# Kernel optimization log

Hardware: AMD Instinct MI355X
Metric: run time of the kernel (lower is better)

The kernel has to match this reference:

```python
import jax, jax.numpy as jnp
import numpy as np

HEADS = 8
DHEAD = 64
KSIZE = 7


def setup_inputs() -> dict:
    key = jax.random.key(0)
    k1, k2, k3, k4 = jax.random.split(key, 4)
    b, H, W, C = 16, 56, 56, 256
    inner = HEADS * DHEAD  # 512
    x = jax.random.normal(k1, (b, H, W, C), jnp.float32)
    Wq = jax.random.normal(k2, (1, 1, C, inner), jnp.float32) * 0.02
    Wkv = jax.random.normal(k3, (KSIZE, KSIZE, C, 2 * inner), jnp.float32) * 0.02
    Wo = jax.random.normal(k4, (1, 1, inner, C), jnp.float32) * 0.02
    bo = jnp.zeros((C,), jnp.float32)
    return {"x": x, "Wq": Wq, "Wkv": Wkv, "Wo": Wo, "bo": bo}


def reference(x, Wq, Wkv, Wo, bo):
    heads, dh = HEADS, DHEAD
    scale = dh ** -0.5
    b, H, W, C = x.shape
    # 1x1 conv Q projection == per-pixel matmul
    q = jnp.einsum('bhwc,cf->bhwf', x, Wq[0, 0])  # [b,H,W,inner]
    # k x k strided conv KV downsample (SAME==VALID since H%k==0)
    kv = jax.lax.conv_general_dilated(
        x, Wkv, window_strides=(KSIZE, KSIZE), padding='VALID',
        dimension_numbers=('NHWC', 'HWIO', 'NHWC'))  # [b,H/k,W/k,2*inner]
    k_, v_ = jnp.split(kv, 2, axis=-1)

    def split_heads(t):
        B, hh, ww, _ = t.shape
        return t.reshape(B, hh * ww, heads, dh)  # [b, seq, h, d]

    q = split_heads(q)      # [b, H*W, h, d]
    k_ = split_heads(k_)    # [b, (H/k)*(W/k), h, d]
    v_ = split_heads(v_)
    dots = jnp.einsum('bqhd,bkhd->bhqk', q, k_) * scale
    attn = jax.nn.softmax(dots, axis=-1)
    out = jnp.einsum('bhqk,bkhd->bqhd', attn, v_)
    out = out.reshape(b, H, W, heads * dh)
    # output 1x1 conv with bias (dropout rate 0 -> identity)
    out = jnp.einsum('bhwf,fc->bhwc', out, Wo[0, 0]) + bo
    return out
```

## Files before the change

### kernel.cpp

```cpp
#include <hip/hip_runtime.h>
#include <stdint.h>

typedef unsigned short ushort_t;
typedef __attribute__((ext_vector_type(8))) unsigned short ushort8v;
typedef __attribute__((ext_vector_type(8))) short short8v;
typedef __attribute__((ext_vector_type(4))) float f32x4;

__device__ __forceinline__ float bf2f(ushort_t u) {
  union { unsigned int i; float f; } v;
  v.i = ((unsigned int)u) << 16;
  return v.f;
}
__device__ __forceinline__ ushort_t f2bf(float f) {
  union { float f; unsigned int i; } v;
  v.f = f;
  unsigned int r = v.i + 0x7FFFu + ((v.i >> 16) & 1u);
  return (ushort_t)(r >> 16);
}

__device__ __forceinline__ ushort8v load8bf(const ushort_t* __restrict__ p) {
  return *(const ushort8v*)p;
}
__device__ __forceinline__ ushort8v load8bf(const float* __restrict__ p) {
  const float4 a = *(const float4*)p;
  const float4 b = *(const float4*)(p + 4);
  ushort8v r;
  r[0] = f2bf(a.x); r[1] = f2bf(a.y); r[2] = f2bf(a.z); r[3] = f2bf(a.w);
  r[4] = f2bf(b.x); r[5] = f2bf(b.y); r[6] = f2bf(b.z); r[7] = f2bf(b.w);
  return r;
}
__device__ __forceinline__ void storeC(float* p, float v) { *p = v; }
__device__ __forceinline__ void storeC(ushort_t* p, float v) { *p = f2bf(v); }

__device__ __forceinline__ size_t pp_off(unsigned g) {
  const unsigned b = g / 3136u;
  const unsigned r = g - b * 3136u;
  const unsigned y = r / 56u, xx = r - y * 56u;
  const unsigned ty = y / 7u, dy = y - ty * 7u;
  const unsigned tx = xx / 7u, dx = xx - tx * 7u;
  return ((size_t)((b * 64u + ty * 8u + tx) * 49u + dy * 7u + dx)) << 8;
}

__global__ __launch_bounds__(256) void transpose_cvt(
    const float* __restrict__ W, ushort_t* __restrict__ WT, int K, int N) {
  __shared__ float tile[32][33];
  const int t = threadIdx.x;
  const int k0 = blockIdx.y * 32;
  const int n0 = blockIdx.x * 32;
  {
    const int r = t >> 3, c4 = (t & 7) * 4;
    const float4 v = *(const float4*)(W + (size_t)(k0 + r) * N + n0 + c4);
    tile[r][c4] = v.x; tile[r][c4 + 1] = v.y;
    tile[r][c4 + 2] = v.z; tile[r][c4 + 3] = v.w;
  }
  __syncthreads();
  {
    const int rn = t >> 3, ck = (t & 7) * 4;
    union { ushort_t u[4]; uint2 v; } o;
#pragma unroll
    for (int j = 0; j < 4; ++j) o.u[j] = f2bf(tile[ck + j][rn]);
    *(uint2*)(WT + (size_t)(n0 + rn) * K + k0 + ck) = o.v;
  }
}

__global__ __launch_bounds__(256) void cvt_f32_bf16(
    const float* __restrict__ in, ushort_t* __restrict__ out) {
  const int i = (blockIdx.x * 256 + threadIdx.x) * 4;
  const float4 v = *(const float4*)(in + i);
  union { ushort_t u[4]; uint2 q; } o;
  o.u[0] = f2bf(v.x); o.u[1] = f2bf(v.y);
  o.u[2] = f2bf(v.z); o.u[3] = f2bf(v.w);
  *(uint2*)(out + i) = o.q;
}

__global__ __launch_bounds__(256) void cvt_im2col(
    const float* __restrict__ x, ushort_t* __restrict__ xp) {
  const int e = (blockIdx.x * 256 + threadIdx.x) * 8;
  const unsigned p = ((unsigned)e) >> 8;
  const int c = e & 255;
  const float4 a = *(const float4*)(x + e);
  const float4 b = *(const float4*)(x + e + 4);
  ushort8v o;
  o[0] = f2bf(a.x); o[1] = f2bf(a.y); o[2] = f2bf(a.z); o[3] = f2bf(a.w);
  o[4] = f2bf(b.x); o[5] = f2bf(b.y); o[6] = f2bf(b.z); o[7] = f2bf(b.w);
  *(ushort8v*)(xp + pp_off(p) + c) = o;
}

template <int MODE, bool PERMA>
__device__ __forceinline__ void gemm_body(
    const ushort_t* __restrict__ A, const ushort_t* __restrict__ BT,
    const float* __restrict__ bias, void* __restrict__ Cv,
    int N, int K, int m0, int n0, int kbeg, int kend) {
  __shared__ ushort_t lA[2][4096];
  __shared__ ushort_t lB[2][4096];
  const int t = threadIdx.x;
  const int lane = t & 63;
  const int wv = t >> 6;
  const int wm = wv >> 1, wn = wv & 1;
  const int sm = t >> 2;
  const int kq = t & 3;

  const int row16 = sm & 15;
  const int wslot = kq * 16 + (row16 ^ kq);
  const int rdsw = (lane ^ ((lane >> 4) & 3)) * 8;

  const ushort_t* aR[2];
  const ushort_t* bR[2];
  int off[2];
#pragma unroll
  for (int h = 0; h < 2; ++h) {
    const int m = h * 64 + sm;
    off[h] = (h * 4 + wv) * 512 + wslot * 8;
    size_t aoff;
    if (PERMA)
      aoff = pp_off((unsigned)(m0 + m));
    else
      aoff = (size_t)(m0 + m) * K;
    aR[h] = A + aoff + kq * 8;
    bR[h] = BT + (size_t)(n0 + m) * K + kq * 8;
  }

  f32x4 acc[4][4] = {};
  const int nst = (kend - kbeg) >> 5;

  ushort8v av[2], bv[2];
#pragma unroll
  for (int h = 0; h < 2; ++h) {
    av[h] = *(const ushort8v*)(aR[h] + kbeg);
    bv[h] = *(const ushort8v*)(bR[h] + kbeg);
  }
#pragma unroll
  for (int h = 0; h < 2; ++h) {
    *(ushort8v*)&lA[0][off[h]] = av[h];
    *(ushort8v*)&lB[0][off[h]] = bv[h];
  }
  __syncthreads();

  for (int st = 0; st < nst; ++st) {
    const int cur = st & 1;
    if (st + 1 < nst) {
      const int nk = kbeg + (st + 1) * 32;
#pragma unroll
      for (int h = 0; h < 2; ++h) {
        av[h] = *(const ushort8v*)(aR[h] + nk);
        bv[h] = *(const ushort8v*)(bR[h] + nk);
      }
    }

    short8v af[4], bfr[4];
#pragma unroll
    for (int i = 0; i < 4; ++i) {
      af[i] = *(const short8v*)&lA[cur][(wm * 4 + i) * 512 + rdsw];
      bfr[i] = *(const short8v*)&lB[cur][(wn * 4 + i) * 512 + rdsw];
    }
#pragma unroll
    for (int i = 0; i < 4; ++i)
#pragma unroll
      for (int j = 0; j < 4; ++j)
        acc[i][j] = __builtin_amdgcn_mfma_f32_16x16x32_bf16(
            af[i], bfr[j], acc[i][j], 0, 0, 0);

    if (st + 1 < nst) {
#pragma unroll
      for (int h = 0; h < 2; ++h) {
        *(ushort8v*)&lA[cur ^ 1][off[h]] = av[h];
        *(ushort8v*)&lB[cur ^ 1][off[h]] = bv[h];
      }
    }
    __syncthreads();
  }

  const int col = lane & 15, rq = (lane >> 4) * 4;
#pragma unroll
  for (int i = 0; i < 4; ++i) {
    const int mb = m0 + (wm * 4 + i) * 16 + rq;
#pragma unroll
    for (int j = 0; j < 4; ++j) {
      const int nb = n0 + (wn * 4 + j) * 16 + col;
      if (MODE == 0) {
        ushort_t* C = (ushort_t*)Cv;
#pragma unroll
        for (int r = 0; r < 4; ++r)
          C[(size_t)(mb + r) * N + nb] = f2bf(acc[i][j][r]);
      } else if (MODE == 1) {
        float* C = (float*)Cv;
        const float badd = bias[nb];
#pragma unroll
        for (int r = 0; r < 4; ++r)
          C[(size_t)(mb + r) * N + nb] = acc[i][j][r] + badd;
      } else {
        float* C = (float*)Cv;
#pragma unroll
        for (int r = 0; r < 4; ++r)
          atomicAdd(&C[(size_t)(mb + r) * N + nb], acc[i][j][r]);
      }
    }
  }
}

template <int MODE, bool PERMA>
__global__ __launch_bounds__(256) void gemm_nt_2d(
    const ushort_t* __restrict__ A, const ushort_t* __restrict__ BT,
    const float* __restrict__ bias, void* __restrict__ C, int N, int K) {
  gemm_body<MODE, PERMA>(A, BT, bias, C, N, K, blockIdx.y * 128,
                         blockIdx.x * 128, 0, K);
}

__global__ __launch_bounds__(256) void gemm_kv_gl(
    const ushort_t* __restrict__ xpat, const ushort_t* __restrict__ WkvT,
    float* __restrict__ C) {
  const int bl = blockIdx.x;
  const int kbeg = (bl >> 6) * 896;
  gemm_body<2, false>(xpat, WkvT, (const float*)nullptr, C, 1024, 12544,
                      (bl & 7) * 128, ((bl >> 3) & 7) * 128, kbeg, kbeg + 896);
}

template <typename TA, typename TC>
__global__ __launch_bounds__(256) void gemm_mfma_nt(
    const TA* __restrict__ A, const ushort_t* __restrict__ BT,
    const float* __restrict__ bias, TC* __restrict__ C,
    int M, int N, int K, int has_bias) {
  __shared__ ushort_t lA[8 * 512];
  __shared__ ushort_t lB[8 * 512];
  const int t = threadIdx.x;
  const int m0 = blockIdx.y * 128;
  const int n0 = blockIdx.x * 128;
  const int lane = t & 63;
  const int wm = (t >> 6) >> 1, wn = (t >> 6) & 1;

  f32x4 acc[4][4] = {};

  const int sm = t >> 2;
  const int kq = t & 3;

  for (int k0 = 0; k0 < K; k0 += 32) {
#pragma unroll
    for (int h = 0; h < 2; ++h) {
      const int m = h * 64 + sm;
      const int off = (m >> 4) * 512 + (kq * 16 + (m & 15)) * 8;
      const ushort8v av = load8bf(A + (size_t)(m0 + m) * K + k0 + kq * 8);
      *(ushort8v*)&lA[off] = av;
      const ushort8v bv = load8bf(BT + (size_t)(n0 + m) * K + k0 + kq * 8);
      *(ushort8v*)&lB[off] = bv;
    }
    __syncthreads();
    short8v af[4], bf[4];
#pragma unroll
    for (int i = 0; i < 4; ++i) {
      af[i] = *(const short8v*)&lA[(wm * 4 + i) * 512 + lane * 8];
      bf[i] = *(const short8v*)&lB[(wn * 4 + i) * 512 + lane * 8];
    }
#pragma unroll
    for (int i = 0; i < 4; ++i)
#pragma unroll
      for (int j = 0; j < 4; ++j)
        acc[i][j] = __builtin_amdgcn_mfma_f32_16x16x32_bf16(
            af[i], bf[j], acc[i][j], 0, 0, 0);
    __syncthreads();
  }

  const int col = lane & 15, rq = (lane >> 4) * 4;
#pragma unroll
  for (int i = 0; i < 4; ++i) {
    const int mb = m0 + (wm * 4 + i) * 16 + rq;
#pragma unroll
    for (int j = 0; j < 4; ++j) {
      const int nb = n0 + (wn * 4 + j) * 16 + col;
      const float badd = has_bias ? bias[nb] : 0.f;
#pragma unroll
      for (int r = 0; r < 4; ++r)
        storeC(&C[(size_t)(mb + r) * N + nb], acc[i][j][r] + badd);
    }
  }
}

template <typename TA>
__global__ __launch_bounds__(256) void gemm_kv_mfma(
    const TA* __restrict__ x, const ushort_t* __restrict__ WkvT,
    float* __restrict__ C) {
  __shared__ ushort_t lA[8 * 512];
  __shared__ ushort_t lB[8 * 512];
  const int t = threadIdx.x;
  const int bl = blockIdx.x;
  const int m0 = (bl & 7) * 128;
  const int n0 = ((bl >> 3) & 7) * 128;
  const int kbeg = (bl >> 6) * 896;
  const int lane = t & 63;
  const int wm = (t >> 6) >> 1, wn = (t >> 6) & 1;

  f32x4 acc[4][4] = {};

  const int sm = t >> 2;
  const int kq = t & 3;

  for (int k0 = kbeg; k0 < kbeg + 896; k0 += 32) {
#pragma unroll
    for (int h = 0; h < 2; ++h) {
      const int m = h * 64 + sm;
      const int off = (m >> 4) * 512 + (kq * 16 + (m & 15)) * 8;
      const int gm = m0 + m;
      const int b = gm >> 6, ty = (gm >> 3) & 7, tx = gm & 7;
      const int k = k0 + kq * 8;
      const int patch = k >> 8;
      const int c = k & 255;
      const int dy = (patch * 37) >> 8;
      const int dx = patch - dy * 7;
      const int pix = b * 3136 + (ty * 7 + dy) * 56 + (tx * 7 + dx);
      const ushort8v av = load8bf(x + (size_t)pix * 256 + c);
      *(ushort8v*)&lA[off] = av;
      const ushort8v bv =
          load8bf(WkvT + (size_t)(n0 + m) * 12544 + k0 + kq * 8);
      *(ushort8v*)&lB[off] = bv;
    }
    __syncthreads();
    short8v af[4], bf[4];
#pragma unroll
    for (int i = 0; i < 4; ++i) {
      af[i] = *(const short8v*)&lA[(wm * 4 + i) * 512 + lane * 8];
      bf[i] = *(const short8v*)&lB[(wn * 4 + i) * 512 + lane * 8];
    }
#pragma unroll
    for (int i = 0; i < 4; ++i)
#pragma unroll
      for (int j = 0; j < 4; ++j)
        acc[i][j] = __builtin_amdgcn_mfma_f32_16x16x32_bf16(
            af[i], bf[j], acc[i][j], 0, 0, 0);
    __syncthreads();
  }

  const int col = lane & 15, rq = (lane >> 4) * 4;
#pragma unroll
  for (int i = 0; i < 4; ++i) {
    const int mb = m0 + (wm * 4 + i) * 16 + rq;
#pragma unroll
    for (int j = 0; j < 4; ++j) {
      const int nb = n0 + (wn * 4 + j) * 16 + col;
#pragma unroll
      for (int r = 0; r < 4; ++r)
        atomicAdd(&C[(size_t)(mb + r) * 1024 + nb], acc[i][j][r]);
    }
  }
}

__global__ __launch_bounds__(256) void attn_mfma(
    ushort_t* __restrict__ qo, const ushort_t* __restrict__ kvb) {
  __shared__ ushort_t VT[64][72];
  __shared__ ushort_t P[4][64][72];
  const int t = threadIdx.x;
  const int lane = t & 63;
  const int w = t >> 6;
  const int bh = blockIdx.y;
  const int b = bh >> 3, h = bh & 7;
  const ushort_t* kvp = kvb + (size_t)(b * 64) * 1024 + h * 64;

  for (int i = t; i < 512; i += 256) {
    const int key = i >> 3, d0 = (i & 7) * 8;
    const ushort8v v = *(const ushort8v*)(kvp + (size_t)key * 1024 + 512 + d0);
#pragma unroll
    for (int jj = 0; jj < 8; ++jj) VT[d0 + jj][key] = v[jj];
  }
  __syncthreads();

  const int q0_raw = blockIdx.x * 256 + w * 64;
  const bool valid = q0_raw < 3136;
  const int q0 = valid ? q0_raw : 3072;
  const size_t qbase = ((size_t)b * 3136 + q0) * 512 + h * 64;

  const int lm = lane & 15, quad = lane >> 4;

  short8v qf[4][2], kf[4][2];
#pragma unroll
  for (int i = 0; i < 4; ++i)
#pragma unroll
    for (int s = 0; s < 2; ++s) {
      qf[i][s] = *(const short8v*)(qo + qbase + (size_t)(16 * i + lm) * 512 +
                                   32 * s + quad * 8);
      kf[i][s] = *(const short8v*)(kvp + (size_t)(16 * i + lm) * 1024 +
                                   32 * s + quad * 8);
    }

  f32x4 sa[4][4];
#pragma unroll
  for (int i = 0; i < 4; ++i)
#pragma unroll
    for (int j = 0; j < 4; ++j) {
      f32x4 z = {};
      z = __builtin_amdgcn_mfma_f32_16x16x32_bf16(qf[i][0], kf[j][0], z, 0, 0, 0);
      sa[i][j] = __builtin_amdgcn_mfma_f32_16x16x32_bf16(qf[i][1], kf[j][1], z, 0, 0, 0);
    }

  float l[4][4];
#pragma unroll
  for (int i = 0; i < 4; ++i)
#pragma unroll
    for (int r = 0; r < 4; ++r) {
      float m = fmaxf(fmaxf(sa[i][0][r], sa[i][1][r]),
                      fmaxf(sa[i][2][r], sa[i][3][r]));
#pragma unroll
      for (int off = 1; off < 16; off <<= 1) m = fmaxf(m, __shfl_xor(m, off));
      float sum = 0.f;
#pragma unroll
      for (int j = 0; j < 4; ++j) {
        const float p = __expf(0.125f * (sa[i][j][r] - m));
        sa[i][j][r] = p;
        sum += p;
      }
#pragma unroll
      for (int off = 1; off < 16; off <<= 1) sum += __shfl_xor(sum, off);
      l[i][r] = sum;
    }

#pragma unroll
  for (int i = 0; i < 4; ++i) {
    const int row = 16 * i + quad * 4;
#pragma unroll
    for (int j = 0; j < 4; ++j) {
      const int col = 16 * j + lm;
#pragma unroll
      for (int r = 0; r < 4; ++r) P[w][row + r][col] = f2bf(sa[i][j][r]);
    }
  }
  __syncthreads();

  short8v vf[4][2];
#pragma unroll
  for (int jn = 0; jn < 4; ++jn)
#pragma unroll
    for (int s2 = 0; s2 < 2; ++s2)
      vf[jn][s2] = *(const short8v*)&VT[16 * jn + lm][32 * s2 + quad * 8];

  f32x4 oa[4][4];
#pragma unroll
  for (int i = 0; i < 4; ++i) {
    const short8v pf0 = *(const short8v*)&P[w][16 * i + lm][quad * 8];
    const short8v pf1 = *(const short8v*)&P[w][16 * i + lm][32 + quad * 8];
#pragma unroll
    for (int jn = 0; jn < 4; ++jn) {
      f32x4 z = {};
      z = __builtin_amdgcn_mfma_f32_16x16x32_bf16(pf0, vf[jn][0], z, 0, 0, 0);
      oa[i][jn] = __builtin_amdgcn_mfma_f32_16x16x32_bf16(pf1, vf[jn][1], z, 0, 0, 0);
    }
  }

  if (valid) {
#pragma unroll
    for (int i = 0; i < 4; ++i) {
#pragma unroll
      for (int r = 0; r < 4; ++r) {
        const float inv = 1.f / l[i][r];
        const size_t rowoff = qbase + (size_t)(16 * i + quad * 4 + r) * 512;
#pragma unroll
        for (int jn = 0; jn < 4; ++jn)
          qo[rowoff + 16 * jn + lm] = f2bf(oa[i][jn][r] * inv);
      }
    }
  }
}

extern "C" void kernel_launch(void* const* d_in, const int* in_sizes, int n_in,
                              void* d_out, int out_size, void* d_ws,
                              size_t ws_size, hipStream_t stream) {
  const float* x = (const float*)d_in[0];
  const float* Wq = (const float*)d_in[1];
  const float* Wkv = (const float*)d_in[2];
  const float* Wo = (const float*)d_in[3];
  const float* bo = (const float*)d_in[4];
  float* out = (float*)d_out;

  char* ws = (char*)d_ws;
  ushort_t* qbuf = (ushort_t*)(ws);
  float* kvbuf = (float*)(ws + 51380224);
  ushort_t* WkvT = (ushort_t*)(ws + 55574528);
  ushort_t* WqT = (ushort_t*)(ws + 81264640);
  ushort_t* WoT = (ushort_t*)(ws + 81526784);
  ushort_t* kvbf = (ushort_t*)(ws + 81788928);
  ushort_t* xpat = (ushort_t*)(ws + 83886080);
  const bool use_fast = ws_size >= 109576192u;

  hipLaunchKernelGGL(transpose_cvt, dim3(16, 8), dim3(256), 0, stream, Wq, WqT,
                     256, 512);
  hipLaunchKernelGGL(transpose_cvt, dim3(32, 392), dim3(256), 0, stream, Wkv,
                     WkvT, 12544, 1024);
  hipLaunchKernelGGL(transpose_cvt, dim3(8, 16), dim3(256), 0, stream, Wo, WoT,
                     512, 256);
  hipMemsetAsync(kvbuf, 0, 1024 * 1024 * 4, stream);

  if (use_fast) {
    hipLaunchKernelGGL(cvt_im2col, dim3(6272), dim3(256), 0, stream, x, xpat);
    hipLaunchKernelGGL((gemm_nt_2d<0, true>), dim3(4, 392), dim3(256), 0,
                       stream, xpat, WqT, (const float*)nullptr, qbuf, 512,
                       256);
    hipLaunchKernelGGL(gemm_kv_gl, dim3(896), dim3(256), 0, stream, xpat,
                       WkvT, kvbuf);
    hipLaunchKernelGGL(cvt_f32_bf16, dim3(1024), dim3(256), 0, stream, kvbuf,
                       kvbf);
    hipLaunchKernelGGL(attn_mfma, dim3(13, 128), dim3(256), 0, stream, qbuf,
                       kvbf);
    hipLaunchKernelGGL((gemm_nt_2d<1, false>), dim3(2, 392), dim3(256), 0,
                       stream, qbuf, WoT, bo, out, 256, 512);
  } else {
    hipLaunchKernelGGL((gemm_mfma_nt<float, ushort_t>), dim3(4, 392),
                       dim3(256), 0, stream, x, WqT, (const float*)nullptr,
                       qbuf, 50176, 512, 256, 0);
    hipLaunchKernelGGL((gemm_kv_mfma<float>), dim3(896), dim3(256), 0, stream,
                       x, WkvT, kvbuf);
    hipLaunchKernelGGL(cvt_f32_bf16, dim3(1024), dim3(256), 0, stream, kvbuf,
                       kvbf);
    hipLaunchKernelGGL(attn_mfma, dim3(13, 128), dim3(256), 0, stream, qbuf,
                       kvbf);
    hipLaunchKernelGGL((gemm_mfma_nt<ushort_t, float>), dim3(2, 392),
                       dim3(256), 0, stream, qbuf, WoT, bo, out, 50176, 256,
                       512, 1);
  }
}
```

Baseline: 343.7 us.

## Deepen GEMM global-load prefetch to two stages ahead with unrolled double buffer

Result: slower. 352.7 us (+2.6%).

```diff
diff --git a/kernel.cpp b/kernel.cpp
--- a/kernel.cpp
+++ b/kernel.cpp
@@ -123,49 +123,92 @@
   f32x4 acc[4][4] = {};
   const int nst = (kend - kbeg) >> 5;
 
-  ushort8v av[2], bv[2];
-#pragma unroll
-  for (int h = 0; h < 2; ++h) {
-    av[h] = *(const ushort8v*)(aR[h] + kbeg);
-    bv[h] = *(const ushort8v*)(bR[h] + kbeg);
-  }
-#pragma unroll
-  for (int h = 0; h < 2; ++h) {
-    *(ushort8v*)&lA[0][off[h]] = av[h];
-    *(ushort8v*)&lB[0][off[h]] = bv[h];
+  ushort8v avA0, avA1, bvA0, bvA1;
+  ushort8v avB0, avB1, bvB0, bvB1;
+
+  {
+    ushort8v a0 = *(const ushort8v*)(aR[0] + kbeg);
+    ushort8v a1 = *(const ushort8v*)(aR[1] + kbeg);
+    ushort8v b0 = *(const ushort8v*)(bR[0] + kbeg);
+    ushort8v b1 = *(const ushort8v*)(bR[1] + kbeg);
+    *(ushort8v*)&lA[0][off[0]] = a0;
+    *(ushort8v*)&lA[0][off[1]] = a1;
+    *(ushort8v*)&lB[0][off[0]] = b0;
+    *(ushort8v*)&lB[0][off[1]] = b1;
+  }
+  if (1 < nst) {
+    const int nk = kbeg + 32;
+    avB0 = *(const ushort8v*)(aR[0] + nk);
+    avB1 = *(const ushort8v*)(aR[1] + nk);
+    bvB0 = *(const ushort8v*)(bR[0] + nk);
+    bvB1 = *(const ushort8v*)(bR[1] + nk);
+  }
+  if (2 < nst) {
+    const int nk = kbeg + 64;
+    avA0 = *(const ushort8v*)(aR[0] + nk);
+    avA1 = *(const ushort8v*)(aR[1] + nk);
+    bvA0 = *(const ushort8v*)(bR[0] + nk);
+    bvA1 = *(const ushort8v*)(bR[1] + nk);
   }
   __syncthreads();
 
-  for (int st = 0; st < nst; ++st) {
-    const int cur = st & 1;
+  for (int st = 0; st < nst; st += 2) {
     if (st + 1 < nst) {
-      const int nk = kbeg + (st + 1) * 32;
-#pragma unroll
-      for (int h = 0; h < 2; ++h) {
-        av[h] = *(const ushort8v*)(aR[h] + nk);
-        bv[h] = *(const ushort8v*)(bR[h] + nk);
+      *(ushort8v*)&lA[1][off[0]] = avB0;
+      *(ushort8v*)&lA[1][off[1]] = avB1;
+      *(ushort8v*)&lB[1][off[0]] = bvB0;
+      *(ushort8v*)&lB[1][off[1]] = bvB1;
+    }
+    if (st + 3 < nst) {
+      const int nk = kbeg + (st + 3) * 32;
+      avB0 = *(const ushort8v*)(aR[0] + nk);
+      avB1 = *(const ushort8v*)(aR[1] + nk);
+      bvB0 = *(const ushort8v*)(bR[0] + nk);
+      bvB1 = *(const ushort8v*)(bR[1] + nk);
+    }
+    {
+      short8v af[4], bfr[4];
+#pragma unroll
+      for (int i = 0; i < 4; ++i) {
+        af[i] = *(const short8v*)&lA[0][(wm * 4 + i) * 512 + rdsw];
+        bfr[i] = *(const short8v*)&lB[0][(wn * 4 + i) * 512 + rdsw];
       }
-    }
-
-    short8v af[4], bfr[4];
-#pragma unroll
-    for (int i = 0; i < 4; ++i) {
-      af[i] = *(const short8v*)&lA[cur][(wm * 4 + i) * 512 + rdsw];
-      bfr[i] = *(const short8v*)&lB[cur][(wn * 4 + i) * 512 + rdsw];
-    }
-#pragma unroll
-    for (int i = 0; i < 4; ++i)
-#pragma unroll
-      for (int j = 0; j < 4; ++j)
-        acc[i][j] = __builtin_amdgcn_mfma_f32_16x16x32_bf16(
-            af[i], bfr[j], acc[i][j], 0, 0, 0);
-
-    if (st + 1 < nst) {
-#pragma unroll
-      for (int h = 0; h < 2; ++h) {
-        *(ushort8v*)&lA[cur ^ 1][off[h]] = av[h];
-        *(ushort8v*)&lB[cur ^ 1][off[h]] = bv[h];
+#pragma unroll
+      for (int i = 0; i < 4; ++i)
+#pragma unroll
+        for (int j = 0; j < 4; ++j)
+          acc[i][j] = __builtin_amdgcn_mfma_f32_16x16x32_bf16(
+              af[i], bfr[j], acc[i][j], 0, 0, 0);
+    }
+    __syncthreads();
+    if (st + 1 >= nst) break;
+
+    if (st + 2 < nst) {
+      *(ushort8v*)&lA[0][off[0]] = avA0;
+      *(ushort8v*)&lA[0][off[1]] = avA1;
+      *(ushort8v*)&lB[0][off[0]] = bvA0;
+      *(ushort8v*)&lB[0][off[1]] = bvA1;
+    }
+    if (st + 4 < nst) {
+      const int nk = kbeg + (st + 4) * 32;
+      avA0 = *(const ushort8v*)(aR[0] + nk);
+      avA1 = *(const ushort8v*)(aR[1] + nk);
+      bvA0 = *(const ushort8v*)(bR[0] + nk);
+      bvA1 = *(const ushort8v*)(bR[1] + nk);
+    }
+    {
+      short8v af[4], bfr[4];
+#pragma unroll
+      for (int i = 0; i < 4; ++i) {
+        af[i] = *(const short8v*)&lA[1][(wm * 4 + i) * 512 + rdsw];
+        bfr[i] = *(const short8v*)&lB[1][(wn * 4 + i) * 512 + rdsw];
       }
+#pragma unroll
+      for (int i = 0; i < 4; ++i)
+#pragma unroll
+        for (int j = 0; j < 4; ++j)
+          acc[i][j] = __builtin_amdgcn_mfma_f32_16x16x32_bf16(
+              af[i], bfr[j], acc[i][j], 0, 0, 0);
     }
     __syncthreads();
   }
```
